# Performance work log

Hardware: AMD Instinct MI355X
Metric: run time of the kernel (lower is better)

## Reference

```python
import jax, jax.numpy as jnp
import numpy as np

D_MODEL = 512
N_HEADS = 8
D_K = D_MODEL // N_HEADS


def setup_inputs() -> dict:
    key = jax.random.key(0)
    ks = jax.random.split(key, 11)
    B, L, D = 2, 4096, D_MODEL
    s = 1.0 / np.sqrt(D)
    return {
        "q": jax.random.normal(ks[0], (B, L, D), jnp.float32),
        "k": jax.random.normal(ks[1], (B, L, D), jnp.float32),
        "v": jax.random.normal(ks[2], (B, L, D), jnp.float32),
        "Wq": jax.random.normal(ks[3], (D, D), jnp.float32) * s,
        "bq": jnp.zeros((D,), jnp.float32),
        "Wk": jax.random.normal(ks[4], (D, D), jnp.float32) * s,
        "bk": jnp.zeros((D,), jnp.float32),
        "Wv": jax.random.normal(ks[5], (D, D), jnp.float32) * s,
        "bv": jnp.zeros((D,), jnp.float32),
        "Wo": jax.random.normal(ks[6], (D, D), jnp.float32) * s,
        "bo": jnp.zeros((D,), jnp.float32),
    }


def reference(q, k, v, Wq, bq, Wk, bk, Wv, bv, Wo, bo):
    B, L, D = q.shape
    H, dk = N_HEADS, D_K
    # projections -> [B, H, L, dk]
    qh = (q @ Wq + bq).reshape(B, L, H, dk).transpose(0, 2, 1, 3)
    kh = (k @ Wk + bk).reshape(B, -1, H, dk).transpose(0, 2, 1, 3)
    vh = (v @ Wv + bv).reshape(B, -1, H, dk).transpose(0, 2, 1, 3)
    scores = jnp.einsum("bhqd,bhkd->bhqk", qh, kh) / jnp.sqrt(jnp.float32(dk))
    attn = jax.nn.softmax(scores, axis=-1)  # dropout: eval-mode identity
    ctx = jnp.einsum("bhqk,bhkd->bhqd", attn, vh)
    ctx = ctx.transpose(0, 2, 1, 3).reshape(B, L, D)
    return ctx @ Wo + bo
```

## Files before the change

### kernel.cpp

```cpp
#include <hip/hip_runtime.h>
#include <hip/hip_bf16.h>

#define NB 2
#define NL 4096
#define ND 512
#define NH 8
#define NDK 64
#define NM (NB * NL)
#define QSCALE 0.18033688011112042f

typedef short bf16x8_t __attribute__((ext_vector_type(8)));
typedef float f32x4_t __attribute__((ext_vector_type(4)));

static __device__ __forceinline__ unsigned short f2bs(float f) {
  union { float f; unsigned u; } c; c.f = f;
  unsigned r = c.u + 0x7fffu + ((c.u >> 16) & 1u);
  return (unsigned short)(r >> 16);
}
static __device__ __forceinline__ float bs2f(unsigned short s) {
  union { unsigned u; float f; } c; c.u = ((unsigned)s) << 16; return c.f;
}
static __device__ __forceinline__ unsigned pk_bf16(float a, float b) {
  union { __hip_bfloat162 h; unsigned u; } c;
  c.h = __float22bfloat162_rn(make_float2(a, b));
  return c.u;
}
static __device__ __forceinline__ unsigned cvt_pk_hw(float a, float b) {
  unsigned r;
  asm("v_cvt_pk_bf16_f32 %0, %1, %2" : "=v"(r) : "v"(a), "v"(b));
  return r;
}

__global__ __launch_bounds__(256)
void round3_kernel(const float* __restrict__ s0, const float* __restrict__ s1,
                   const float* __restrict__ s2, unsigned short* __restrict__ d0,
                   unsigned short* __restrict__ d1, unsigned short* __restrict__ d2)
{
  const float* s = blockIdx.y == 0 ? s0 : (blockIdx.y == 1 ? s1 : s2);
  unsigned short* d = blockIdx.y == 0 ? d0 : (blockIdx.y == 1 ? d1 : d2);
  const size_t i = ((size_t)blockIdx.x * 256 + threadIdx.x) * 8;
  const float4 f0 = *(const float4*)(s + i);
  const float4 f1 = *(const float4*)(s + i + 4);
  uint4 o;
  o.x = pk_bf16(f0.x, f0.y);
  o.y = pk_bf16(f0.z, f0.w);
  o.z = pk_bf16(f1.x, f1.y);
  o.w = pk_bf16(f1.z, f1.w);
  *(uint4*)(d + i) = o;
}

struct WArgs {
  const float* W[4];
  unsigned short* Th[4];
  unsigned short* Tl[4];
};
__global__ __launch_bounds__(256)
void wsplit_kernel(WArgs a)
{
  const int z = blockIdx.z;
  const float* __restrict__ W = a.W[z];
  const int tid = threadIdx.x;
  const int n = blockIdx.x * 64 + (tid & 63);
  const int kb = blockIdx.y * 64 + (tid >> 6) * 16;
  unsigned short h[16], l[16];
#pragma unroll
  for (int u = 0; u < 16; ++u) {
    const float x = W[(size_t)(kb + u) * ND + n];
    h[u] = f2bs(x);
    l[u] = f2bs(x - bs2f(h[u]));
  }
  unsigned wh[8], wl[8];
#pragma unroll
  for (int p = 0; p < 8; ++p) {
    wh[p] = (unsigned)h[2 * p] | ((unsigned)h[2 * p + 1] << 16);
    wl[p] = (unsigned)l[2 * p] | ((unsigned)l[2 * p + 1] << 16);
  }
  unsigned short* th = a.Th[z] + (size_t)n * ND + kb;
  unsigned short* tl = a.Tl[z] + (size_t)n * ND + kb;
  *(uint4*)th = make_uint4(wh[0], wh[1], wh[2], wh[3]);
  *(uint4*)(th + 8) = make_uint4(wh[4], wh[5], wh[6], wh[7]);
  *(uint4*)tl = make_uint4(wl[0], wl[1], wl[2], wl[3]);
  *(uint4*)(tl + 8) = make_uint4(wl[4], wl[5], wl[6], wl[7]);
}

template <bool ASPLIT, int NJ, int OUTMODE>
__device__ __forceinline__ void gemm_core(
    const unsigned short* __restrict__ Ahi, const unsigned short* __restrict__ Alo,
    const unsigned short* __restrict__ Bh, const unsigned short* __restrict__ Bl,
    const float* __restrict__ bias, unsigned short* __restrict__ outH,
    float* __restrict__ outF, int m0, int n0, float scale)
{
  __shared__ unsigned short AH[128][36];
  __shared__ unsigned short AL[ASPLIT ? 128 : 1][36];
  __shared__ unsigned short BHs[NJ * 16][36];
  __shared__ unsigned short BLs[NJ * 16][36];

  const int tid = threadIdx.x;
  const int lane = tid & 63, w = tid >> 6;
  const int m = lane & 15, quad = lane >> 4;
  const int r = tid >> 1, hf = (tid & 1) * 16;
  const int rb = (NJ == 8) ? (tid >> 1) : (tid >> 2);
  const int cb = (NJ == 8) ? ((tid & 1) * 16) : ((tid & 3) * 8);

  const unsigned short* aRow = Ahi + (size_t)(m0 + r) * ND + hf;
  const unsigned short* alRow = ASPLIT ? (Alo + (size_t)(m0 + r) * ND + hf) : nullptr;
  const unsigned short* bhRow = Bh + (size_t)(n0 + rb) * ND + cb;
  const unsigned short* blRow = Bl + (size_t)(n0 + rb) * ND + cb;

  uint4 ra0 = *(const uint4*)(aRow);
  uint4 ra1 = *(const uint4*)(aRow + 8);
  uint4 rl0, rl1;
  if constexpr (ASPLIT) {
    rl0 = *(const uint4*)(alRow);
    rl1 = *(const uint4*)(alRow + 8);
  }
  uint4 rbh0 = *(const uint4*)(bhRow);
  uint4 rbl0 = *(const uint4*)(blRow);
  uint4 rbh1, rbl1;
  if constexpr (NJ == 8) {
    rbh1 = *(const uint4*)(bhRow + 8);
    rbl1 = *(const uint4*)(blRow + 8);
  }

  f32x4_t acc[2][NJ];
#pragma unroll
  for (int i = 0; i < 2; ++i)
#pragma unroll
    for (int j = 0; j < NJ; ++j) acc[i][j] = (f32x4_t){0.f, 0.f, 0.f, 0.f};

  for (int k0 = 0; k0 < ND; k0 += 32) {
    __syncthreads();
    *(uint4*)&AH[r][hf] = ra0;
    *(uint4*)&AH[r][hf + 8] = ra1;
    if constexpr (ASPLIT) {
      *(uint4*)&AL[r][hf] = rl0;
      *(uint4*)&AL[r][hf + 8] = rl1;
    }
    *(uint4*)&BHs[rb][cb] = rbh0;
    *(uint4*)&BLs[rb][cb] = rbl0;
    if constexpr (NJ == 8) {
      *(uint4*)&BHs[rb][cb + 8] = rbh1;
      *(uint4*)&BLs[rb][cb + 8] = rbl1;
    }
    if (k0 + 32 < ND) {
      const int kn = k0 + 32;
      ra0 = *(const uint4*)(aRow + kn);
      ra1 = *(const uint4*)(aRow + kn + 8);
      if constexpr (ASPLIT) {
        rl0 = *(const uint4*)(alRow + kn);
        rl1 = *(const uint4*)(alRow + kn + 8);
      }
      rbh0 = *(const uint4*)(bhRow + kn);
      rbl0 = *(const uint4*)(blRow + kn);
      if constexpr (NJ == 8) {
        rbh1 = *(const uint4*)(bhRow + kn + 8);
        rbl1 = *(const uint4*)(blRow + kn + 8);
      }
    }
    __syncthreads();

    bf16x8_t ah[2], al[2];
#pragma unroll
    for (int i = 0; i < 2; ++i) {
      ah[i] = *(const bf16x8_t*)&AH[w * 32 + 16 * i + m][quad * 8];
      if constexpr (ASPLIT) al[i] = *(const bf16x8_t*)&AL[w * 32 + 16 * i + m][quad * 8];
    }
#pragma unroll
    for (int j = 0; j < NJ; ++j) {
      const bf16x8_t bhj = *(const bf16x8_t*)&BHs[16 * j + m][quad * 8];
      const bf16x8_t blj = *(const bf16x8_t*)&BLs[16 * j + m][quad * 8];
#pragma unroll
      for (int i = 0; i < 2; ++i) {
        acc[i][j] = __builtin_amdgcn_mfma_f32_16x16x32_bf16(ah[i], bhj, acc[i][j], 0, 0, 0);
        acc[i][j] = __builtin_amdgcn_mfma_f32_16x16x32_bf16(ah[i], blj, acc[i][j], 0, 0, 0);
        if constexpr (ASPLIT)
          acc[i][j] = __builtin_amdgcn_mfma_f32_16x16x32_bf16(al[i], bhj, acc[i][j], 0, 0, 0);
      }
    }
  }

  if constexpr (OUTMODE != 2) {
#pragma unroll
    for (int i = 0; i < 2; ++i)
#pragma unroll
      for (int rr = 0; rr < 4; ++rr) {
        const int mg = m0 + w * 32 + 16 * i + quad * 4 + rr;
#pragma unroll
        for (int j = 0; j < NJ; ++j) {
          const int n = n0 + 16 * j + m;
          const float c = (acc[i][j][rr] + bias[n]) * scale;
          if constexpr (OUTMODE == 0) {
            const int b = mg >> 12, l = mg & (NL - 1);
            const int h = n >> 6, d = n & (NDK - 1);
            outH[(((size_t)(b * NH + h)) * NL + l) * NDK + d] = f2bs(c);
          } else {
            outF[(size_t)mg * ND + n] = c;
          }
        }
      }
  } else {
    unsigned short* T = &BHs[0][0];
    const int bb = m0 >> 12;
    const int lbase = m0 & (NL - 1);
#pragma unroll 1
    for (int p = 0; p < 4; ++p) {
      __syncthreads();
      if (w == p) {
#pragma unroll
        for (int i = 0; i < 2; ++i)
#pragma unroll
          for (int j = 0; j < NJ; ++j) {
            const int n = 16 * j + m;
            const float bv = bias[n0 + n];
            const unsigned w0 = pk_bf16((acc[i][j][0] + bv) * scale,
                                        (acc[i][j][1] + bv) * scale);
            const unsigned w1 = pk_bf16((acc[i][j][2] + bv) * scale,
                                        (acc[i][j][3] + bv) * scale);
            *(uint2*)&T[n * 34 + 16 * i + quad * 4] = make_uint2(w0, w1);
          }
      }
      __syncthreads();
      const int n = tid >> 1;
      const int l0 = (tid & 1) * 16;
      const uint4 t0 = *(const uint4*)&T[n * 34 + l0];
      const uint4 t1 = *(const uint4*)&T[n * 34 + l0 + 8];
      const int ng = n0 + n;
      const int h = ng >> 6, d = ng & (NDK - 1);
      unsigned short* dp =
          outH + (((size_t)(bb * NH + h)) * NDK + d) * NL + lbase + 32 * p + l0;
      *(uint4*)dp = t0;
      *(uint4*)(dp + 8) = t1;
    }
  }
}

struct ProjArgs {
  const unsigned short* A[3];
  const unsigned short* Bh[3];
  const unsigned short* Bl[3];
  const float* bias[3];
  unsigned short* out[3];
  float scale[3];
};
__global__ __launch_bounds__(256, 3)
void gemm_proj_kernel(ProjArgs a)
{
  const int z = blockIdx.z;
  if (z < 2)
    gemm_core<false, 8, 0>(a.A[z], nullptr, a.Bh[z], a.Bl[z], a.bias[z], a.out[z],
                           nullptr, blockIdx.x * 128, blockIdx.y * 128, a.scale[z]);
  else
    gemm_core<false, 8, 2>(a.A[2], nullptr, a.Bh[2], a.Bl[2], a.bias[2], a.out[2],
                           nullptr, blockIdx.x * 128, blockIdx.y * 128, a.scale[2]);
}
__global__ __launch_bounds__(256, 3)
void gemm_out_kernel(const unsigned short* __restrict__ Ahi,
                     const unsigned short* __restrict__ Alo,
                     const unsigned short* __restrict__ Bh,
                     const unsigned short* __restrict__ Bl,
                     const float* __restrict__ bias, float* __restrict__ out)
{
  gemm_core<true, 4, 1>(Ahi, Alo, Bh, Bl, bias, nullptr, out,
                        blockIdx.x * 128, blockIdx.y * 64, 1.0f);
}

__global__ __launch_bounds__(256, 2)
void attn_kernel(const unsigned short* __restrict__ qh, const unsigned short* __restrict__ kh,
                 const unsigned short* __restrict__ vt_g, float* __restrict__ op,
                 float* __restrict__ lp)
{
  __shared__ unsigned short Ks[64 * 64];
  __shared__ unsigned short Vt[64 * 64];

  const int tid = threadIdx.x;
  const int w = tid >> 6;
  const int lane = tid & 63;
  const int m = lane & 15;
  const int quad = lane >> 4;
  const int sw = m & 7;

  const int bid = blockIdx.x;
  const int half = bid & 1;
  const int qt = (bid >> 1) & 15;
  const int bh = bid >> 5;
  const int kt0 = half * 32, kt1 = kt0 + 32;
  const unsigned short* qb = qh + (size_t)bh * NL * NDK;
  const unsigned short* kb = kh + (size_t)bh * NL * NDK;
  const unsigned short* vb = vt_g + (size_t)bh * NDK * NL;

  bf16x8_t aq[4][2];
#pragma unroll
  for (int mt = 0; mt < 4; ++mt) {
    const unsigned short* qsrc =
        qb + (size_t)(qt * 256 + w * 64 + mt * 16 + m) * NDK + quad * 8;
    aq[mt][0] = *(const bf16x8_t*)(qsrc);
    aq[mt][1] = *(const bf16x8_t*)(qsrc + 32);
  }

  const short ob = (short)0x3F80;
  const bf16x8_t ones = {ob, ob, ob, ob, ob, ob, ob, ob};

  f32x4_t o[4][4];
#pragma unroll
  for (int mt = 0; mt < 4; ++mt)
#pragma unroll
    for (int nt = 0; nt < 4; ++nt) o[mt][nt] = (f32x4_t){0.f, 0.f, 0.f, 0.f};
  f32x4_t ol[4];
#pragma unroll
  for (int mt = 0; mt < 4; ++mt) ol[mt] = (f32x4_t){0.f, 0.f, 0.f, 0.f};

  const int kr = tid >> 2;
  const int kcb = tid & 3;
  const int kc = kcb * 16;
  const int r7 = kr & 7;
  const int st0 = kr * 64 + ((2 * kcb) ^ r7) * 8;
  const int st1 = kr * 64 + ((2 * kcb + 1) ^ r7) * 8;

  const int rowb = m * 64;
  const int ck0 = rowb + ((quad ^ sw) * 8);
  const int ck1 = rowb + (((quad + 4) ^ sw) * 8);
  const int vq = quad >> 1, vo = (quad & 1) * 4;
  const int va0[2] = { rowb + vo + (((0 + vq) ^ sw) * 8),
                       rowb + vo + (((4 + vq) ^ sw) * 8) };
  const int va1[2] = { rowb + vo + (((2 + vq) ^ sw) * 8),
                       rowb + vo + (((6 + vq) ^ sw) * 8) };

  const unsigned short* kptr = kb + (size_t)(kt0 * 64 + kr) * NDK + kc;
  const unsigned short* vptr = vb + (size_t)kr * NL + kt0 * 64 + kc;
  uint4 pk0 = *(const uint4*)kptr;
  uint4 pk1 = *(const uint4*)(kptr + 8);
  uint4 pv0 = *(const uint4*)vptr;
  uint4 pv1 = *(const uint4*)(vptr + 8);

  for (int kt = kt0; kt < kt1; ++kt) {
    __syncthreads();
    *(uint4*)&Ks[st0] = pk0;
    *(uint4*)&Ks[st1] = pk1;
    *(uint4*)&Vt[st0] = pv0;
    *(uint4*)&Vt[st1] = pv1;
    if (kt + 1 < kt1) {
      kptr += 64 * NDK;
      vptr += 64;
      pk0 = *(const uint4*)kptr;
      pk1 = *(const uint4*)(kptr + 8);
      pv0 = *(const uint4*)vptr;
      pv1 = *(const uint4*)(vptr + 8);
    }
    __syncthreads();

#pragma unroll
    for (int c = 0; c < 2; ++c) {
      unsigned paw[4][4];
#pragma unroll
      for (int t = 0; t < 2; ++t) {
        const int nt = 2 * c + t;
        const bf16x8_t kf0 = *(const bf16x8_t*)&Ks[nt * 1024 + ck0];
        const bf16x8_t kf1 = *(const bf16x8_t*)&Ks[nt * 1024 + ck1];
#pragma unroll
        for (int mt = 0; mt < 4; ++mt) {
          f32x4_t s = (f32x4_t){0.f, 0.f, 0.f, 0.f};
          s = __builtin_amdgcn_mfma_f32_16x16x32_bf16(kf0, aq[mt][0], s, 0, 0, 0);
          s = __builtin_amdgcn_mfma_f32_16x16x32_bf16(kf1, aq[mt][1], s, 0, 0, 0);
          paw[mt][2 * t]     = cvt_pk_hw(__builtin_amdgcn_exp2f(s[0]),
                                         __builtin_amdgcn_exp2f(s[1]));
          paw[mt][2 * t + 1] = cvt_pk_hw(__builtin_amdgcn_exp2f(s[2]),
                                         __builtin_amdgcn_exp2f(s[3]));
        }
      }
      union U { bf16x8_t v; unsigned d[4]; };
      U pa[4];
#pragma unroll
      for (int mt = 0; mt < 4; ++mt) {
        pa[mt].d[0] = paw[mt][0];
        pa[mt].d[1] = paw[mt][1];
        pa[mt].d[2] = paw[mt][2];
        pa[mt].d[3] = paw[mt][3];
      }
      __builtin_amdgcn_s_setprio(1);
#pragma unroll
      for (int nt = 0; nt < 4; ++nt) {
        union { bf16x8_t v; uint2 h[2]; } vf;
        vf.h[0] = *(const uint2*)&Vt[nt * 1024 + va0[c]];
        vf.h[1] = *(const uint2*)&Vt[nt * 1024 + va1[c]];
#pragma unroll
        for (int mt = 0; mt < 4; ++mt)
          o[mt][nt] = __builtin_amdgcn_mfma_f32_16x16x32_bf16(pa[mt].v, vf.v, o[mt][nt], 0, 0, 0);
      }
#pragma unroll
      for (int mt = 0; mt < 4; ++mt)
        ol[mt] = __builtin_amdgcn_mfma_f32_16x16x32_bf16(pa[mt].v, ones, ol[mt], 0, 0, 0);
      __builtin_amdgcn_s_setprio(0);
    }
  }

  const size_t pbase = (size_t)(half * 16 + bh) * NL;
#pragma unroll
  for (int mt = 0; mt < 4; ++mt) {
    const int q0 = qt * 256 + w * 64 + mt * 16 + quad * 4;
    if (m == 0)
      *(float4*)&lp[pbase + q0] =
          make_float4(ol[mt][0], ol[mt][1], ol[mt][2], ol[mt][3]);
#pragma unroll
    for (int r = 0; r < 4; ++r) {
      float* dst = op + (pbase + q0 + r) * NDK;
#pragma unroll
      for (int nt = 0; nt < 4; ++nt) dst[16 * nt + m] = o[mt][nt][r];
    }
  }
}

__global__ __launch_bounds__(256)
void merge_kernel(const float* __restrict__ op, const float* __restrict__ lp,
                  unsigned short* __restrict__ ctxh, unsigned short* __restrict__ ctxl)
{
  const size_t t = (size_t)blockIdx.x * 256 + threadIdx.x;
  const int d0 = (int)(t & 7) * 8;
  const size_t row = t >> 3;
  const float l0 = lp[row];
  const float l1 = lp[row + (size_t)16 * NL];
  const float inv = 1.0f / (l0 + l1);
  const float* a = op + row * NDK + d0;
  const float* c = a + (size_t)16 * NL * NDK;
  const float4 a0 = *(const float4*)a, a1 = *(const float4*)(a + 4);
  const float4 c0 = *(const float4*)c, c1 = *(const float4*)(c + 4);
  const float x[8] = {(a0.x + c0.x) * inv, (a0.y + c0.y) * inv,
                      (a0.z + c0.z) * inv, (a0.w + c0.w) * inv,
                      (a1.x + c1.x) * inv, (a1.y + c1.y) * inv,
                      (a1.z + c1.z) * inv, (a1.w + c1.w) * inv};
  unsigned short hs[8], ls[8];
#pragma unroll
  for (int u = 0; u < 8; ++u) {
    hs[u] = f2bs(x[u]);
    ls[u] = f2bs(x[u] - bs2f(hs[u]));
  }
  const int bh = (int)(row >> 12), l = (int)(row & (NL - 1));
  const int b = bh >> 3, h = bh & 7;
  const size_t dst = ((size_t)(b * NL + l)) * ND + h * 64 + d0;
  uint4 uh, ul;
  uh.x = (unsigned)hs[0] | ((unsigned)hs[1] << 16);
  uh.y = (unsigned)hs[2] | ((unsigned)hs[3] << 16);
  uh.z = (unsigned)hs[4] | ((unsigned)hs[5] << 16);
  uh.w = (unsigned)hs[6] | ((unsigned)hs[7] << 16);
  ul.x = (unsigned)ls[0] | ((unsigned)ls[1] << 16);
  ul.y = (unsigned)ls[2] | ((unsigned)ls[3] << 16);
  ul.z = (unsigned)ls[4] | ((unsigned)ls[5] << 16);
  ul.w = (unsigned)ls[6] | ((unsigned)ls[7] << 16);
  *(uint4*)(ctxh + dst) = uh;
  *(uint4*)(ctxl + dst) = ul;
}

extern "C" void kernel_launch(void* const* d_in, const int* in_sizes, int n_in,
                              void* d_out, int out_size, void* d_ws, size_t ws_size,
                              hipStream_t stream)
{
  const float* q  = (const float*)d_in[0];
  const float* k  = (const float*)d_in[1];
  const float* v  = (const float*)d_in[2];
  const float* Wq = (const float*)d_in[3];
  const float* bq = (const float*)d_in[4];
  const float* Wk = (const float*)d_in[5];
  const float* bk = (const float*)d_in[6];
  const float* Wv = (const float*)d_in[7];
  const float* bv = (const float*)d_in[8];
  const float* Wo = (const float*)d_in[9];
  const float* bo = (const float*)d_in[10];

  const size_t PLANE = (size_t)NM * ND;
  unsigned short* wt = (unsigned short*)d_ws;
  unsigned short* qhp = wt + 8 * (size_t)ND * ND;
  unsigned short* khp = qhp + PLANE;
  unsigned short* vtp = khp + PLANE;
  float* op = (float*)(vtp + PLANE);
  float* lp = op + 2 * (size_t)16 * NL * NDK;
  unsigned short* qb = (unsigned short*)op;
  unsigned short* kb = qb + PLANE;
  unsigned short* vb = kb + PLANE;
  unsigned short* ctxh = qhp;
  unsigned short* ctxl = khp;

  unsigned short* wth[4], *wtl[4];
  for (int i = 0; i < 4; ++i) {
    wth[i] = wt + (size_t)(2 * i) * ND * ND;
    wtl[i] = wt + (size_t)(2 * i + 1) * ND * ND;
  }

  round3_kernel<<<dim3(PLANE / (256 * 8), 3), 256, 0, stream>>>(q, k, v, qb, kb, vb);

  WArgs wa;
  wa.W[0] = Wq; wa.W[1] = Wk; wa.W[2] = Wv; wa.W[3] = Wo;
  for (int i = 0; i < 4; ++i) { wa.Th[i] = wth[i]; wa.Tl[i] = wtl[i]; }
  wsplit_kernel<<<dim3(8, 8, 4), 256, 0, stream>>>(wa);

  ProjArgs pa;
  pa.A[0] = qb; pa.A[1] = kb; pa.A[2] = vb;
  pa.Bh[0] = wth[0]; pa.Bl[0] = wtl[0];
  pa.Bh[1] = wth[1]; pa.Bl[1] = wtl[1];
  pa.Bh[2] = wth[2]; pa.Bl[2] = wtl[2];
  pa.bias[0] = bq; pa.bias[1] = bk; pa.bias[2] = bv;
  pa.out[0] = qhp; pa.out[1] = khp; pa.out[2] = vtp;
  pa.scale[0] = QSCALE; pa.scale[1] = 1.0f; pa.scale[2] = 1.0f;
  gemm_proj_kernel<<<dim3(NM / 128, ND / 128, 3), 256, 0, stream>>>(pa);

  attn_kernel<<<dim3(NB * NH * (NL / 256) * 2), 256, 0, stream>>>(qhp, khp, vtp, op, lp);

  merge_kernel<<<dim3((16 * NL * NDK) / (256 * 8)), 256, 0, stream>>>(op, lp, ctxh, ctxl);

  gemm_out_kernel<<<dim3(NM / 128, ND / 64), 256, 0, stream>>>(
      ctxh, ctxl, wth[3], wtl[3], bo, (float*)d_out);
}
```

Measured before the change: 243.1 us.

## Double-buffer K/V tiles in attention and stage QKV head-layout stores through LDS

The attention loop now uses two LDS buffers for the K and V tiles, writing the next tile while the current one is consumed, so each iteration needs one barrier instead of two. Separately, the OUTMODE 0 projection epilogue (head-major bf16 output) stages results through shared memory and writes 16-byte vectors instead of scattered 2-byte stores. This doubles the attention kernel's LDS footprint, which could affect occupancy, and adds barriers to the projection epilogue.

```diff
diff --git a/kernel.cpp b/kernel.cpp
--- a/kernel.cpp
+++ b/kernel.cpp
@@ -179,7 +179,7 @@
     }
   }
 
-  if constexpr (OUTMODE != 2) {
+  if constexpr (OUTMODE == 1) {
 #pragma unroll
     for (int i = 0; i < 2; ++i)
 #pragma unroll
@@ -188,16 +188,40 @@
 #pragma unroll
         for (int j = 0; j < NJ; ++j) {
           const int n = n0 + 16 * j + m;
-          const float c = (acc[i][j][rr] + bias[n]) * scale;
-          if constexpr (OUTMODE == 0) {
-            const int b = mg >> 12, l = mg & (NL - 1);
-            const int h = n >> 6, d = n & (NDK - 1);
-            outH[(((size_t)(b * NH + h)) * NL + l) * NDK + d] = f2bs(c);
-          } else {
-            outF[(size_t)mg * ND + n] = c;
-          }
+          outF[(size_t)mg * ND + n] = (acc[i][j][rr] + bias[n]) * scale;
         }
       }
+  } else if constexpr (OUTMODE == 0) {
+    unsigned short* T = &BHs[0][0];
+    const int bb = m0 >> 12;
+#pragma unroll 1
+    for (int p = 0; p < 4; ++p) {
+      __syncthreads();
+      if (w == p) {
+#pragma unroll
+        for (int i = 0; i < 2; ++i)
+#pragma unroll
+          for (int j = 0; j < NJ; ++j) {
+            const int n = 16 * j + m;
+            const float bv = bias[n0 + n];
+#pragma unroll
+            for (int rr = 0; rr < 4; ++rr)
+              T[(16 * i + quad * 4 + rr) * 136 + n] =
+                  f2bs((acc[i][j][rr] + bv) * scale);
+          }
+      }
+      __syncthreads();
+      const int lr = tid >> 3;
+      const int seg = tid & 7;
+      const uint4 t0 = *(const uint4*)&T[lr * 136 + seg * 16];
+      const uint4 t1 = *(const uint4*)&T[lr * 136 + seg * 16 + 8];
+      const int ng = n0 + seg * 16;
+      const int h = ng >> 6, d = ng & (NDK - 1);
+      const int l = (m0 + p * 32 + lr) & (NL - 1);
+      unsigned short* dp = outH + (((size_t)(bb * NH + h)) * NL + l) * NDK + d;
+      *(uint4*)dp = t0;
+      *(uint4*)(dp + 8) = t1;
+    }
   } else {
     unsigned short* T = &BHs[0][0];
     const int bb = m0 >> 12;
@@ -269,8 +293,8 @@
                  const unsigned short* __restrict__ vt_g, float* __restrict__ op,
                  float* __restrict__ lp)
 {
-  __shared__ unsigned short Ks[64 * 64];
-  __shared__ unsigned short Vt[64 * 64];
+  __shared__ unsigned short Ks[2][64 * 64];
+  __shared__ unsigned short Vt[2][64 * 64];
 
   const int tid = threadIdx.x;
   const int w = tid >> 6;
@@ -331,67 +355,87 @@
   uint4 pk1 = *(const uint4*)(kptr + 8);
   uint4 pv0 = *(const uint4*)vptr;
   uint4 pv1 = *(const uint4*)(vptr + 8);
-
-  for (int kt = kt0; kt < kt1; ++kt) {
-    __syncthreads();
-    *(uint4*)&Ks[st0] = pk0;
-    *(uint4*)&Ks[st1] = pk1;
-    *(uint4*)&Vt[st0] = pv0;
-    *(uint4*)&Vt[st1] = pv1;
-    if (kt + 1 < kt1) {
-      kptr += 64 * NDK;
-      vptr += 64;
-      pk0 = *(const uint4*)kptr;
-      pk1 = *(const uint4*)(kptr + 8);
-      pv0 = *(const uint4*)vptr;
-      pv1 = *(const uint4*)(vptr + 8);
-    }
-    __syncthreads();
-
-#pragma unroll
-    for (int c = 0; c < 2; ++c) {
-      unsigned paw[4][4];
-#pragma unroll
-      for (int t = 0; t < 2; ++t) {
-        const int nt = 2 * c + t;
-        const bf16x8_t kf0 = *(const bf16x8_t*)&Ks[nt * 1024 + ck0];
-        const bf16x8_t kf1 = *(const bf16x8_t*)&Ks[nt * 1024 + ck1];
-#pragma unroll
-        for (int mt = 0; mt < 4; ++mt) {
-          f32x4_t s = (f32x4_t){0.f, 0.f, 0.f, 0.f};
-          s = __builtin_amdgcn_mfma_f32_16x16x32_bf16(kf0, aq[mt][0], s, 0, 0, 0);
-          s = __builtin_amdgcn_mfma_f32_16x16x32_bf16(kf1, aq[mt][1], s, 0, 0, 0);
-          paw[mt][2 * t]     = cvt_pk_hw(__builtin_amdgcn_exp2f(s[0]),
-                                         __builtin_amdgcn_exp2f(s[1]));
-          paw[mt][2 * t + 1] = cvt_pk_hw(__builtin_amdgcn_exp2f(s[2]),
-                                         __builtin_amdgcn_exp2f(s[3]));
-        }
-      }
-      union U { bf16x8_t v; unsigned d[4]; };
-      U pa[4];
-#pragma unroll
-      for (int mt = 0; mt < 4; ++mt) {
-        pa[mt].d[0] = paw[mt][0];
-        pa[mt].d[1] = paw[mt][1];
-        pa[mt].d[2] = paw[mt][2];
-        pa[mt].d[3] = paw[mt][3];
-      }
-      __builtin_amdgcn_s_setprio(1);
-#pragma unroll
-      for (int nt = 0; nt < 4; ++nt) {
-        union { bf16x8_t v; uint2 h[2]; } vf;
-        vf.h[0] = *(const uint2*)&Vt[nt * 1024 + va0[c]];
-        vf.h[1] = *(const uint2*)&Vt[nt * 1024 + va1[c]];
-#pragma unroll
-        for (int mt = 0; mt < 4; ++mt)
-          o[mt][nt] = __builtin_amdgcn_mfma_f32_16x16x32_bf16(pa[mt].v, vf.v, o[mt][nt], 0, 0, 0);
-      }
-#pragma unroll
-      for (int mt = 0; mt < 4; ++mt)
-        ol[mt] = __builtin_amdgcn_mfma_f32_16x16x32_bf16(pa[mt].v, ones, ol[mt], 0, 0, 0);
-      __builtin_amdgcn_s_setprio(0);
-    }
-  }
+  *(uint4*)&Ks[0][st0] = pk0;
+  *(uint4*)&Ks[0][st1] = pk1;
+  *(uint4*)&Vt[0][st0] = pv0;
+  *(uint4*)&Vt[0][st1] = pv1;
+  kptr += 64 * NDK;
+  vptr += 64;
+  pk0 = *(const uint4*)kptr;
+  pk1 = *(const uint4*)(kptr + 8);
+  pv0 = *(const uint4*)vptr;
+  pv1 = *(const uint4*)(vptr + 8);
+  __syncthreads();
+
+#define ATTN_STEP(B, W, KT)                                                   \
+  {                                                                           \
+    _Pragma("unroll")                                                         \
+    for (int c = 0; c < 2; ++c) {                                             \
+      unsigned paw[4][4];                                                     \
+      _Pragma("unroll")                                                       \
+      for (int t = 0; t < 2; ++t) {                                           \
+        const int nt = 2 * c + t;                                             \
+        const bf16x8_t kf0 = *(const bf16x8_t*)&Ks[B][nt * 1024 + ck0];       \
+        const bf16x8_t kf1 = *(const bf16x8_t*)&Ks[B][nt * 1024 + ck1];       \
+        _Pragma("unroll")                                                     \
+        for (int mt = 0; mt < 4; ++mt) {                                      \
+          f32x4_t s = (f32x4_t){0.f, 0.f, 0.f, 0.f};                          \
+          s = __builtin_amdgcn_mfma_f32_16x16x32_bf16(kf0, aq[mt][0], s, 0, 0, 0); \
+          s = __builtin_amdgcn_mfma_f32_16x16x32_bf16(kf1, aq[mt][1], s, 0, 0, 0); \
+          paw[mt][2 * t]     = cvt_pk_hw(__builtin_amdgcn_exp2f(s[0]),        \
+                                         __builtin_amdgcn_exp2f(s[1]));       \
+          paw[mt][2 * t + 1] = cvt_pk_hw(__builtin_amdgcn_exp2f(s[2]),        \
+                                         __builtin_amdgcn_exp2f(s[3]));       \
+        }                                                                     \
+      }                                                                       \
+      union U { bf16x8_t v; unsigned d[4]; };                                 \
+      U pa[4];                                                                \
+      _Pragma("unroll")                                                       \
+      for (int mt = 0; mt < 4; ++mt) {                                        \
+        pa[mt].d[0] = paw[mt][0];                                             \
+        pa[mt].d[1] = paw[mt][1];                                             \
+        pa[mt].d[2] = paw[mt][2];                                             \
+        pa[mt].d[3] = paw[mt][3];                                             \
+      }                                                                       \
+      __builtin_amdgcn_s_setprio(1);                                          \
+      _Pragma("unroll")                                                       \
+      for (int nt = 0; nt < 4; ++nt) {                                        \
+        union { bf16x8_t v; uint2 h[2]; } vf;                                 \
+        vf.h[0] = *(const uint2*)&Vt[B][nt * 1024 + va0[c]];                  \
+        vf.h[1] = *(const uint2*)&Vt[B][nt * 1024 + va1[c]];                  \
+        _Pragma("unroll")                                                     \
+        for (int mt = 0; mt < 4; ++mt)                                        \
+          o[mt][nt] = __builtin_amdgcn_mfma_f32_16x16x32_bf16(pa[mt].v, vf.v, \
+                                                              o[mt][nt], 0, 0, 0); \
+      }                                                                       \
+      _Pragma("unroll")                                                       \
+      for (int mt = 0; mt < 4; ++mt)                                          \
+        ol[mt] = __builtin_amdgcn_mfma_f32_16x16x32_bf16(pa[mt].v, ones,      \
+                                                         ol[mt], 0, 0, 0);    \
+      __builtin_amdgcn_s_setprio(0);                                          \
+    }                                                                         \
+    if ((KT) + 1 < kt1) {                                                     \
+      *(uint4*)&Ks[W][st0] = pk0;                                             \
+      *(uint4*)&Ks[W][st1] = pk1;                                             \
+      *(uint4*)&Vt[W][st0] = pv0;                                             \
+      *(uint4*)&Vt[W][st1] = pv1;                                             \
+      if ((KT) + 2 < kt1) {                                                   \
+        kptr += 64 * NDK;                                                     \
+        vptr += 64;                                                           \
+        pk0 = *(const uint4*)kptr;                                            \
+        pk1 = *(const uint4*)(kptr + 8);                                      \
+        pv0 = *(const uint4*)vptr;                                            \
+        pv1 = *(const uint4*)(vptr + 8);                                      \
+      }                                                                       \
+      __syncthreads();                                                        \
+    }                                                                         \
+  }
+
+  for (int kt = kt0; kt < kt1; kt += 2) {
+    ATTN_STEP(0, 1, kt);
+    ATTN_STEP(1, 0, kt + 1);
+  }
+#undef ATTN_STEP
 
   const size_t pbase = (size_t)(half * 16 + bh) * NL;
 #pragma unroll
```

Result: no change. 242.7 us (-0.2%).
